# Optimization experiments

Measured on AMD Instinct MI355X. Metric: run time of the kernel, lower is better.

The kernel has to match this reference:

```python
import jax, jax.numpy as jnp
import numpy as np

HEAD_NUM = 16
KEY_DIM = 64
EMBED = 1024
KV_OUT = HEAD_NUM * KEY_DIM  # 1024


def setup_inputs() -> dict:
    key = jax.random.key(0)
    ks = jax.random.split(key, 11)
    B, L, E = 2, 2048, EMBED
    scale = 0.02
    return {
        "query": jax.random.normal(ks[0], (B, L, E), jnp.float32),
        "key": jax.random.normal(ks[1], (B, L, E), jnp.float32),
        "value": jax.random.normal(ks[2], (B, L, E), jnp.float32),
        "W_Query": jax.random.normal(ks[3], (E, KV_OUT), jnp.float32) * scale,
        "W_Key": jax.random.normal(ks[4], (E, KV_OUT), jnp.float32) * scale,
        "W_Value": jax.random.normal(ks[5], (E, KV_OUT), jnp.float32) * scale,
        "W_Output": jax.random.normal(ks[6], (KV_OUT, E), jnp.float32) * scale,
        "B_Query": jnp.zeros((KV_OUT,), jnp.float32),
        "B_Key": jnp.zeros((KV_OUT,), jnp.float32),
        "B_Value": jnp.zeros((KV_OUT,), jnp.float32),
        "B_Output": jnp.zeros((E,), jnp.float32),
    }


def reference(query, key, value, W_Query, W_Key, W_Value, W_Output,
              B_Query, B_Key, B_Value, B_Output):
    B, Lq, E = query.shape
    Lk = key.shape[1]
    H, D = HEAD_NUM, KEY_DIM
    # QKV projections + bias
    q = query @ W_Query + B_Query            # [B, Lq, H*D]
    k = key @ W_Key + B_Key                  # [B, Lk, H*D]
    v = value @ W_Value + B_Value            # [B, Lk, H*D]
    # tf.split(axis=2) per head == reshape to [B, L, H, D]
    q = q.reshape(B, Lq, H, D)
    k = k.reshape(B, Lk, H, D)
    v = v.reshape(B, Lk, H, D)
    # scaled dot-product attention (no mask, dropout=0)
    scores = jnp.einsum("bqhd,bkhd->bhqk", q, k) / (D ** 0.5)
    probs = jax.nn.softmax(scores, axis=-1)
    out = jnp.einsum("bhqk,bkhd->bqhd", probs, v)  # [B, Lq, H, D]
    out = out.reshape(B, Lq, H * D)
    return out @ W_Output + B_Output
```

## Files before the change

### kernel.cpp

```cpp
#include <hip/hip_runtime.h>

using u16 = unsigned short;
using u32 = unsigned int;

typedef __attribute__((ext_vector_type(8))) short bf16x8;
typedef __attribute__((ext_vector_type(4))) float f32x4;
typedef __attribute__((ext_vector_type(4))) u32 u32x4;
typedef __attribute__((ext_vector_type(2))) u32 u32x2;
typedef __attribute__((ext_vector_type(4))) _Float16 f16x4;

#define MFMA_BF16_K32(a, b, c) __builtin_amdgcn_mfma_f32_16x16x32_bf16((a), (b), (c), 0, 0, 0)
#define MFMA_F16_K16(a, b, c) __builtin_amdgcn_mfma_f32_16x16x16f16((a), (b), (c), 0, 0, 0)

#define QSCALE 0.18033688011112042f

extern "C" __device__ float __ocml_native_exp2_f32(float);

__device__ __forceinline__ u16 f2bf(float f) {
  u32 u = __builtin_bit_cast(u32, f);
  return (u16)((u + 0x7fffu + ((u >> 16) & 1u)) >> 16);
}

__device__ __forceinline__ u32 pk_f16(float a, float b) {
  auto v = __builtin_amdgcn_cvt_pkrtz(a, b);
  return __builtin_bit_cast(u32, v);
}

__device__ __forceinline__ void load_lds16(const void* g, void* l) {
  __builtin_amdgcn_global_load_lds((__attribute__((address_space(1))) void*)g,
                                   (__attribute__((address_space(3))) void*)l,
                                   16, 0, 0);
}

__global__ __launch_bounds__(256) void cvt_all_kernel(
    const float* __restrict__ q, const float* __restrict__ k, const float* __restrict__ v,
    u16* __restrict__ oq, u16* __restrict__ ok, u16* __restrict__ ov,
    const float* __restrict__ w0, const float* __restrict__ w1,
    const float* __restrict__ w2, const float* __restrict__ w3,
    u16* __restrict__ d0, u16* __restrict__ d1,
    u16* __restrict__ d2, u16* __restrict__ d3) {
  const int id = blockIdx.x;
  const int tid = threadIdx.x;
  if (id < 6144) {
    const int z = id >> 11, bx = id & 2047;
    const float* s = z == 0 ? q : z == 1 ? k : v;
    u16* d = z == 0 ? oq : z == 1 ? ok : ov;
    int i = (bx * 256 + tid) * 8;
    f32x4 a = *(const f32x4*)(s + i);
    f32x4 b = *(const f32x4*)(s + i + 4);
    u32x4 o;
    o.x = (u32)f2bf(a.x) | ((u32)f2bf(a.y) << 16);
    o.y = (u32)f2bf(a.z) | ((u32)f2bf(a.w) << 16);
    o.z = (u32)f2bf(b.x) | ((u32)f2bf(b.y) << 16);
    o.w = (u32)f2bf(b.z) | ((u32)f2bf(b.w) << 16);
    *(u32x4*)(d + i) = o;
    return;
  }
  __shared__ float t[64][65];
  const int r0 = id - 6144;
  const int z = r0 >> 8, rr0 = r0 & 255;
  const int bx = rr0 & 15, by = rr0 >> 4;
  const float* src = z == 0 ? w0 : z == 1 ? w1 : z == 2 ? w2 : w3;
  u16* dst = z == 0 ? d0 : z == 1 ? d1 : z == 2 ? d2 : d3;
  const float scale = (z == 0) ? QSCALE : 1.0f;
  const int r = tid >> 4, c4 = (tid & 15) * 4;
#pragma unroll
  for (int i = 0; i < 4; ++i) {
    int row = r + i * 16;
    f32x4 vv = *(const f32x4*)(src + (by * 64 + row) * 1024 + bx * 64 + c4);
    t[row][c4 + 0] = vv.x;
    t[row][c4 + 1] = vv.y;
    t[row][c4 + 2] = vv.z;
    t[row][c4 + 3] = vv.w;
  }
  __syncthreads();
  const int rw = tid >> 2, cc = (tid & 3) * 16;
  alignas(16) u16 tmp[16];
#pragma unroll
  for (int j = 0; j < 16; ++j) tmp[j] = f2bf(t[cc + j][rw] * scale);
  u32x4* outp = (u32x4*)(dst + (bx * 64 + rw) * 1024 + by * 64 + cc);
  outp[0] = *(const u32x4*)&tmp[0];
  outp[1] = *(const u32x4*)&tmp[8];
}

__global__ __launch_bounds__(256) void gemm_qkv_kernel(
    const u16* __restrict__ x0, const u16* __restrict__ x1, const u16* __restrict__ x2,
    const u16* __restrict__ w0, const u16* __restrict__ w1, const u16* __restrict__ w2,
    const float* __restrict__ b0, const float* __restrict__ b1, const float* __restrict__ b2,
    u16* __restrict__ c0, u16* __restrict__ c1, u16* __restrict__ vt) {
  __shared__ u16 As[128 * 64];
  __shared__ u16 Bs[128 * 64];
  const int lid = blockIdx.x;
  const int xcd = lid & 7, rr = lid >> 3;
  const int nb = rr & 7, slot = rr >> 3;
  const int g = slot * 8 + xcd;
  const int z = g >> 5, m_idx = g & 31;
  const u16* A = z == 0 ? x0 : z == 1 ? x1 : x2;
  const u16* Bt = z == 0 ? w0 : z == 1 ? w1 : w2;
  const float* bias = z == 0 ? b0 : z == 1 ? b1 : b2;
  const float bscale = z == 0 ? QSCALE : 1.0f;
  const int tid = threadIdx.x;
  const int wave = tid >> 6, lane = tid & 63;
  const int l16 = lane & 15, quad = lane >> 4;
  const int l7 = l16 & 7;
  const int wm = wave >> 1, wn = wave & 1;
  const int m0 = m_idx * 128, n0 = nb * 128;

  f32x4 acc[4][4];
  const f32x4 zf = {0.f, 0.f, 0.f, 0.f};
#pragma unroll
  for (int i = 0; i < 4; ++i)
#pragma unroll
    for (int j = 0; j < 4; ++j) acc[i][j] = zf;

  for (int kb = 0; kb < 1024; kb += 64) {
#pragma unroll
    for (int t = 0; t < 4; ++t) {
      int c = wave * 256 + t * 64 + lane;
      int row = c >> 3, sc8 = (c & 7) ^ (row & 7);
      load_lds16(A + (m0 + row) * 1024 + kb + sc8 * 8, &As[(wave * 256 + t * 64) * 8]);
    }
#pragma unroll
    for (int t = 0; t < 4; ++t) {
      int c = wave * 256 + t * 64 + lane;
      int row = c >> 3, sc8 = (c & 7) ^ (row & 7);
      load_lds16(Bt + (n0 + row) * 1024 + kb + sc8 * 8, &Bs[(wave * 256 + t * 64) * 8]);
    }
    asm volatile("s_waitcnt vmcnt(0)" ::: "memory");
    __syncthreads();
#pragma unroll
    for (int ks = 0; ks < 2; ++ks) {
      const int sch = (ks * 4 + quad) ^ l7;
      bf16x8 af[4], bfv[4];
#pragma unroll
      for (int mt = 0; mt < 4; ++mt)
        af[mt] = *(const bf16x8*)&As[(wm * 64 + mt * 16 + l16) * 64 + sch * 8];
#pragma unroll
      for (int nt = 0; nt < 4; ++nt)
        bfv[nt] = *(const bf16x8*)&Bs[(wn * 64 + nt * 16 + l16) * 64 + sch * 8];
#pragma unroll
      for (int mt = 0; mt < 4; ++mt)
#pragma unroll
        for (int nt = 0; nt < 4; ++nt) acc[mt][nt] = MFMA_BF16_K32(af[mt], bfv[nt], acc[mt][nt]);
    }
    __syncthreads();
  }

  float bv[4];
#pragma unroll
  for (int nt = 0; nt < 4; ++nt) bv[nt] = bias[n0 + wn * 64 + nt * 16 + l16] * bscale;
  if (z != 2) {
    u16* C = z == 0 ? c0 : c1;
#pragma unroll
    for (int mt = 0; mt < 4; ++mt)
#pragma unroll
      for (int nt = 0; nt < 4; ++nt)
#pragma unroll
        for (int r = 0; r < 4; ++r) {
          int row = m0 + wm * 64 + mt * 16 + quad * 4 + r;
          int col = n0 + wn * 64 + nt * 16 + l16;
          C[row * 1024 + col] = f2bf(acc[mt][nt][r] + bv[nt]);
        }
  } else {
#pragma unroll
    for (int mt = 0; mt < 4; ++mt)
#pragma unroll
      for (int nt = 0; nt < 4; ++nt)
#pragma unroll
        for (int r = 0; r < 4; ++r) {
          int row = m0 + wm * 64 + mt * 16 + quad * 4 + r;
          int col = n0 + wn * 64 + nt * 16 + l16;
          int bb = row >> 11, kv = row & 2047;
          _Float16 hv = (_Float16)(acc[mt][nt][r] + bv[nt]);
          vt[(bb * 1024 + col) * 2048 + kv] = __builtin_bit_cast(u16, hv);
        }
  }
}

__global__ __launch_bounds__(256) void gemm_out_kernel(const u16* __restrict__ A,
                                                       const u16* __restrict__ Bt,
                                                       const float* __restrict__ bias,
                                                       float* __restrict__ C) {
  __shared__ u16 As[64 * 64];
  __shared__ u16 Bs[128 * 64];
  const int lid = blockIdx.x;
  const int xcd = lid & 7, rr = lid >> 3;
  const int nb = rr & 7, slot = rr >> 3;
  const int by = slot * 8 + xcd;
  const int tid = threadIdx.x;
  const int wave = tid >> 6, lane = tid & 63;
  const int l16 = lane & 15, quad = lane >> 4;
  const int l7 = l16 & 7;
  const int m0 = by * 64, n0 = nb * 128;

  f32x4 acc[4][2];
  const f32x4 zf = {0.f, 0.f, 0.f, 0.f};
#pragma unroll
  for (int i = 0; i < 4; ++i)
#pragma unroll
    for (int j = 0; j < 2; ++j) acc[i][j] = zf;

  for (int kb = 0; kb < 1024; kb += 64) {
#pragma unroll
    for (int t = 0; t < 2; ++t) {
      int c = wave * 128 + t * 64 + lane;
      int row = c >> 3, sc8 = (c & 7) ^ (row & 7);
      load_lds16(A + (m0 + row) * 1024 + kb + sc8 * 8, &As[(wave * 128 + t * 64) * 8]);
    }
#pragma unroll
    for (int t = 0; t < 4; ++t) {
      int c = wave * 256 + t * 64 + lane;
      int row = c >> 3, sc8 = (c & 7) ^ (row & 7);
      load_lds16(Bt + (n0 + row) * 1024 + kb + sc8 * 8, &Bs[(wave * 256 + t * 64) * 8]);
    }
    asm volatile("s_waitcnt vmcnt(0)" ::: "memory");
    __syncthreads();
#pragma unroll
    for (int ks = 0; ks < 2; ++ks) {
      const int sch = (ks * 4 + quad) ^ l7;
      bf16x8 af[4], bfv[2];
#pragma unroll
      for (int mt = 0; mt < 4; ++mt)
        af[mt] = *(const bf16x8*)&As[(mt * 16 + l16) * 64 + sch * 8];
#pragma unroll
      for (int nt = 0; nt < 2; ++nt)
        bfv[nt] = *(const bf16x8*)&Bs[(wave * 32 + nt * 16 + l16) * 64 + sch * 8];
#pragma unroll
      for (int mt = 0; mt < 4; ++mt)
#pragma unroll
        for (int nt = 0; nt < 2; ++nt) acc[mt][nt] = MFMA_BF16_K32(af[mt], bfv[nt], acc[mt][nt]);
    }
    __syncthreads();
  }

  float bv[2];
#pragma unroll
  for (int nt = 0; nt < 2; ++nt) bv[nt] = bias[n0 + wave * 32 + nt * 16 + l16];
#pragma unroll
  for (int mt = 0; mt < 4; ++mt)
#pragma unroll
    for (int nt = 0; nt < 2; ++nt)
#pragma unroll
      for (int r = 0; r < 4; ++r) {
        int row = m0 + mt * 16 + quad * 4 + r;
        int col = n0 + wave * 32 + nt * 16 + l16;
        C[row * 1024 + col] = acc[mt][nt][r] + bv[nt];
      }
}

__global__ __launch_bounds__(256, 2) void flash_kernel(const u16* __restrict__ Q,
                                                       const u16* __restrict__ K,
                                                       const u16* __restrict__ Vt,
                                                       u16* __restrict__ O) {
  __shared__ u16 k_lds[2][128 * 64];
  __shared__ u16 vt_lds[2][64 * 128];
  __shared__ float lred[4][64];
  __shared__ float lfin[64];
  const int tid = threadIdx.x;
  const int wave = tid >> 6, lane = tid & 63;
  const int l16 = lane & 15, quad = lane >> 4;
  const int l7 = l16 & 7;
  const int id = blockIdx.x;
  const int xcd = id & 7, slot = id >> 3;
  const int pair = xcd * 4 + (slot & 3);
  const int qb = slot >> 2;
  const int b = pair >> 4, h = pair & 15;
  const u16* Qh = Q + (b * 2048 + qb * 64) * 1024 + h * 64;
  const u16* Kh = K + b * 2048 * 1024 + h * 64;
  const u16* Vh = Vt + pair * 64 * 2048;

#pragma unroll
  for (int t = 0; t < 2; ++t) {
    int c = (t * 4 + wave) * 64 + lane;
    int row = c >> 3, sc8 = (c & 7) ^ (row & 7);
    load_lds16(Qh + row * 1024 + sc8 * 8, &k_lds[0][((t * 4 + wave) * 64) * 8]);
  }
  asm volatile("s_waitcnt vmcnt(0)" ::: "memory");
  __syncthreads();
  bf16x8 qf[4][2];
#pragma unroll
  for (int qn = 0; qn < 4; ++qn)
#pragma unroll
    for (int ks = 0; ks < 2; ++ks)
      qf[qn][ks] = *(const bf16x8*)&k_lds[0][(qn * 16 + l16) * 64 + (((ks * 4 + quad) ^ l7)) * 8];
  __syncthreads();

#pragma unroll
  for (int bufi = 0; bufi < 2; ++bufi) {
    const int kv0 = bufi * 128;
#pragma unroll
    for (int t = 0; t < 4; ++t) {
      int c = (t * 4 + wave) * 64 + lane;
      int row = c >> 3, sc8 = (c & 7) ^ (row & 7);
      load_lds16(Kh + (kv0 + row) * 1024 + sc8 * 8, &k_lds[bufi][((t * 4 + wave) * 64) * 8]);
    }
#pragma unroll
    for (int t = 0; t < 4; ++t) {
      int c = (t * 4 + wave) * 64 + lane;
      int d = c >> 4, sc = (c & 15) ^ (d & 15);
      load_lds16(Vh + d * 2048 + kv0 + sc * 8, &vt_lds[bufi][((t * 4 + wave) * 64) * 8]);
    }
  }

  f32x4 o_acc[4][4];
  const f32x4 zf = {0.f, 0.f, 0.f, 0.f};
#pragma unroll
  for (int qn = 0; qn < 4; ++qn)
#pragma unroll
    for (int dt = 0; dt < 4; ++dt) o_acc[qn][dt] = zf;
  float lp[4] = {0.f, 0.f, 0.f, 0.f};

  for (int kb = 0; kb < 16; ++kb) {
    const int cur = kb & 1;
    if (kb < 15)
      asm volatile("s_waitcnt vmcnt(8)" ::: "memory");
    else
      asm volatile("s_waitcnt vmcnt(0)" ::: "memory");
    __builtin_amdgcn_s_barrier();
    asm volatile("" ::: "memory");

#pragma unroll
    for (int c2 = 0; c2 < 2; ++c2) {
      const int chunk = wave * 2 + c2;
      f32x4 s_acc[4];
#pragma unroll
      for (int qn = 0; qn < 4; ++qn) s_acc[qn] = zf;
#pragma unroll
      for (int ks = 0; ks < 2; ++ks) {
        bf16x8 kf =
            *(const bf16x8*)&k_lds[cur][(chunk * 16 + l16) * 64 + ((ks * 4 + quad) ^ l7) * 8];
        __builtin_amdgcn_s_setprio(1);
#pragma unroll
        for (int qn = 0; qn < 4; ++qn) s_acc[qn] = MFMA_BF16_K32(kf, qf[qn][ks], s_acc[qn]);
        __builtin_amdgcn_s_setprio(0);
      }
      union { u32 u[2]; f16x4 v; } pkv[4];
#pragma unroll
      for (int qn = 0; qn < 4; ++qn) {
        float e0 = __ocml_native_exp2_f32(s_acc[qn].x);
        float e1 = __ocml_native_exp2_f32(s_acc[qn].y);
        float e2 = __ocml_native_exp2_f32(s_acc[qn].z);
        float e3 = __ocml_native_exp2_f32(s_acc[qn].w);
        lp[qn] += (e0 + e1) + (e2 + e3);
        pkv[qn].u[0] = pk_f16(e0, e1);
        pkv[qn].u[1] = pk_f16(e2, e3);
      }
#pragma unroll
      for (int dt = 0; dt < 4; ++dt) {
        f16x4 vf = *(const f16x4*)&vt_lds[cur][(dt * 16 + l16) * 128 +
                                               (((chunk * 2 + (quad >> 1)) ^ l16) * 8) +
                                               (quad & 1) * 4];
        __builtin_amdgcn_s_setprio(1);
#pragma unroll
        for (int qn = 0; qn < 4; ++qn)
          o_acc[qn][dt] = MFMA_F16_K16(pkv[qn].v, vf, o_acc[qn][dt]);
        __builtin_amdgcn_s_setprio(0);
      }
    }

    __builtin_amdgcn_s_barrier();
    asm volatile("" ::: "memory");
    if (kb + 2 < 16) {
      const int kv0 = (kb + 2) * 128;
#pragma unroll
      for (int t = 0; t < 4; ++t) {
        int c = (t * 4 + wave) * 64 + lane;
        int row = c >> 3, sc8 = (c & 7) ^ (row & 7);
        load_lds16(Kh + (kv0 + row) * 1024 + sc8 * 8, &k_lds[cur][((t * 4 + wave) * 64) * 8]);
      }
#pragma unroll
      for (int t = 0; t < 4; ++t) {
        int c = (t * 4 + wave) * 64 + lane;
        int d = c >> 4, sc = (c & 15) ^ (d & 15);
        load_lds16(Vh + d * 2048 + kv0 + sc * 8, &vt_lds[cur][((t * 4 + wave) * 64) * 8]);
      }
    }
  }

#pragma unroll
  for (int qn = 0; qn < 4; ++qn) {
    lp[qn] += __shfl_xor(lp[qn], 16);
    lp[qn] += __shfl_xor(lp[qn], 32);
  }
  if (quad == 0) {
#pragma unroll
    for (int qn = 0; qn < 4; ++qn) lred[wave][qn * 16 + l16] = lp[qn];
  }
  float* bufA = (float*)&k_lds[0][0];
  float* bufB = (float*)&k_lds[1][0];
  if (wave == 1 || wave == 3) {
    float* buf = (wave == 1) ? bufA : bufB;
#pragma unroll
    for (int qm = 0; qm < 4; ++qm)
#pragma unroll
      for (int dt = 0; dt < 4; ++dt)
        *(f32x4*)&buf[(((qm * 4 + dt) * 4 + quad) * 16 + l16) * 4] = o_acc[qm][dt];
  }
  __syncthreads();
  if (tid < 64) lfin[tid] = lred[0][tid] + lred[1][tid] + lred[2][tid] + lred[3][tid];
  if (wave == 0 || wave == 2) {
    float* buf = (wave == 0) ? bufA : bufB;
#pragma unroll
    for (int qm = 0; qm < 4; ++qm)
#pragma unroll
      for (int dt = 0; dt < 4; ++dt)
        o_acc[qm][dt] += *(const f32x4*)&buf[(((qm * 4 + dt) * 4 + quad) * 16 + l16) * 4];
  }
  __syncthreads();
  if (wave == 2) {
#pragma unroll
    for (int qm = 0; qm < 4; ++qm)
#pragma unroll
      for (int dt = 0; dt < 4; ++dt)
        *(f32x4*)&bufA[(((qm * 4 + dt) * 4 + quad) * 16 + l16) * 4] = o_acc[qm][dt];
  }
  __syncthreads();
  if (wave == 0) {
#pragma unroll
    for (int qm = 0; qm < 4; ++qm)
#pragma unroll
      for (int dt = 0; dt < 4; ++dt)
        o_acc[qm][dt] += *(const f32x4*)&bufA[(((qm * 4 + dt) * 4 + quad) * 16 + l16) * 4];
#pragma unroll
    for (int qm = 0; qm < 4; ++qm)
#pragma unroll
      for (int r = 0; r < 4; ++r) {
        int qrow = qm * 16 + quad * 4 + r;
        float inv = 1.0f / lfin[qrow];
        int row = b * 2048 + qb * 64 + qrow;
#pragma unroll
        for (int dt = 0; dt < 4; ++dt)
          O[row * 1024 + h * 64 + dt * 16 + l16] = f2bf(o_acc[qm][dt][r] * inv);
      }
  }
}

extern "C" void kernel_launch(void* const* d_in, const int* in_sizes, int n_in,
                              void* d_out, int out_size, void* d_ws, size_t ws_size,
                              hipStream_t stream) {
  const float* q = (const float*)d_in[0];
  const float* k = (const float*)d_in[1];
  const float* v = (const float*)d_in[2];
  const float* Wq = (const float*)d_in[3];
  const float* Wk = (const float*)d_in[4];
  const float* Wv = (const float*)d_in[5];
  const float* Wo = (const float*)d_in[6];
  const float* Bq = (const float*)d_in[7];
  const float* Bk = (const float*)d_in[8];
  const float* Bv = (const float*)d_in[9];
  const float* Bo = (const float*)d_in[10];
  float* out = (float*)d_out;

  char* w = (char*)d_ws;
  const size_t MB = 1u << 20;
  u16* xq = (u16*)(w + 0 * MB);
  u16* xk = (u16*)(w + 8 * MB);
  u16* xv = (u16*)(w + 16 * MB);
  u16* wqt = (u16*)(w + 24 * MB);
  u16* wkt = (u16*)(w + 26 * MB);
  u16* wvt = (u16*)(w + 28 * MB);
  u16* wot = (u16*)(w + 30 * MB);
  u16* Qp = (u16*)(w + 32 * MB);
  u16* Kp = (u16*)(w + 40 * MB);
  u16* Vtr = (u16*)(w + 48 * MB);
  u16* At = (u16*)(w + 56 * MB);

  cvt_all_kernel<<<dim3(7168), 256, 0, stream>>>(q, k, v, xq, xk, xv,
                                                 Wq, Wk, Wv, Wo, wqt, wkt, wvt, wot);
  gemm_qkv_kernel<<<dim3(768), 256, 0, stream>>>(xq, xk, xv, wqt, wkt, wvt,
                                                 Bq, Bk, Bv, Qp, Kp, Vtr);
  flash_kernel<<<dim3(1024), 256, 0, stream>>>(Qp, Kp, Vtr, At);
  gemm_out_kernel<<<dim3(512), 256, 0, stream>>>(At, wot, Bo, out);
}
```

Measured before the change: 231.2 us.

## Pre-tile V^T into MFMA fragment layout and load V directly to registers

The V projection epilogue now writes V^T in a blocked layout that matches the flash kernel's MFMA B-operand fragments, using vectorized 4-element f16 stores. The flash kernel drops the V LDS double buffer and loads V fragments straight from global memory into registers at the start of each KV block, deferring the PV MFMAs until after the next K prefetch is issued. This cuts LDS traffic and capacity and may raise occupancy, at the cost of exposed global-load latency for V within each iteration and more live registers.

```diff
diff --git a/kernel.cpp b/kernel.cpp
--- a/kernel.cpp
+++ b/kernel.cpp
@@ -165,15 +165,19 @@
 #pragma unroll
     for (int mt = 0; mt < 4; ++mt)
 #pragma unroll
-      for (int nt = 0; nt < 4; ++nt)
-#pragma unroll
-        for (int r = 0; r < 4; ++r) {
-          int row = m0 + wm * 64 + mt * 16 + quad * 4 + r;
-          int col = n0 + wn * 64 + nt * 16 + l16;
-          int bb = row >> 11, kv = row & 2047;
-          _Float16 hv = (_Float16)(acc[mt][nt][r] + bv[nt]);
-          vt[(bb * 1024 + col) * 2048 + kv] = __builtin_bit_cast(u16, hv);
-        }
+      for (int nt = 0; nt < 4; ++nt) {
+        int kvb = m0 + wm * 64 + mt * 16 + quad * 4;
+        int bb = kvb >> 11, kv = kvb & 2047;
+        int col = n0 + wn * 64 + nt * 16 + l16;
+        int h = col >> 6, dt = (col >> 4) & 3, ld = col & 15;
+        int pair = bb * 16 + h;
+        int kb2 = kv >> 7, chunk = (kv >> 4) & 7, qd = (kv >> 2) & 3;
+        f16x4 hv;
+#pragma unroll
+        for (int r = 0; r < 4; ++r) hv[r] = (_Float16)(acc[mt][nt][r] + bv[nt]);
+        u16* dst = vt + ((((pair * 16 + kb2) * 8 + chunk) * 4 + dt) * 256) + qd * 64 + ld * 4;
+        *(f16x4*)dst = hv;
+      }
   }
 }
 
@@ -253,7 +257,6 @@
                                                        const u16* __restrict__ Vt,
                                                        u16* __restrict__ O) {
   __shared__ u16 k_lds[2][128 * 64];
-  __shared__ u16 vt_lds[2][64 * 128];
   __shared__ float lred[4][64];
   __shared__ float lfin[64];
   const int tid = threadIdx.x;
@@ -267,7 +270,7 @@
   const int b = pair >> 4, h = pair & 15;
   const u16* Qh = Q + (b * 2048 + qb * 64) * 1024 + h * 64;
   const u16* Kh = K + b * 2048 * 1024 + h * 64;
-  const u16* Vh = Vt + pair * 64 * 2048;
+  const u16* Vh = Vt + pair * 131072;
 
 #pragma unroll
   for (int t = 0; t < 2; ++t) {
@@ -287,18 +290,12 @@
 
 #pragma unroll
   for (int bufi = 0; bufi < 2; ++bufi) {
-    const int kv0 = bufi * 128;
 #pragma unroll
     for (int t = 0; t < 4; ++t) {
       int c = (t * 4 + wave) * 64 + lane;
       int row = c >> 3, sc8 = (c & 7) ^ (row & 7);
-      load_lds16(Kh + (kv0 + row) * 1024 + sc8 * 8, &k_lds[bufi][((t * 4 + wave) * 64) * 8]);
-    }
-#pragma unroll
-    for (int t = 0; t < 4; ++t) {
-      int c = (t * 4 + wave) * 64 + lane;
-      int d = c >> 4, sc = (c & 15) ^ (d & 15);
-      load_lds16(Vh + d * 2048 + kv0 + sc * 8, &vt_lds[bufi][((t * 4 + wave) * 64) * 8]);
+      load_lds16(Kh + (bufi * 128 + row) * 1024 + sc8 * 8,
+                 &k_lds[bufi][((t * 4 + wave) * 64) * 8]);
     }
   }
 
@@ -312,13 +309,21 @@
 
   for (int kb = 0; kb < 16; ++kb) {
     const int cur = kb & 1;
-    if (kb < 15)
-      asm volatile("s_waitcnt vmcnt(8)" ::: "memory");
-    else
-      asm volatile("s_waitcnt vmcnt(0)" ::: "memory");
+    if (kb == 0) asm volatile("s_waitcnt vmcnt(4)" ::: "memory");
     __builtin_amdgcn_s_barrier();
     asm volatile("" ::: "memory");
 
+    const u16* vp = Vh + kb * 8192;
+    f16x4 vreg[2][4];
+#pragma unroll
+    for (int c2 = 0; c2 < 2; ++c2) {
+      const int chunk = wave * 2 + c2;
+#pragma unroll
+      for (int dt = 0; dt < 4; ++dt)
+        vreg[c2][dt] = *(const f16x4*)(vp + (chunk * 4 + dt) * 256 + lane * 4);
+    }
+
+    union { u32 u[2]; f16x4 v; } pkv[2][4];
 #pragma unroll
     for (int c2 = 0; c2 < 2; ++c2) {
       const int chunk = wave * 2 + c2;
@@ -334,7 +339,6 @@
         for (int qn = 0; qn < 4; ++qn) s_acc[qn] = MFMA_BF16_K32(kf, qf[qn][ks], s_acc[qn]);
         __builtin_amdgcn_s_setprio(0);
       }
-      union { u32 u[2]; f16x4 v; } pkv[4];
 #pragma unroll
       for (int qn = 0; qn < 4; ++qn) {
         float e0 = __ocml_native_exp2_f32(s_acc[qn].x);
@@ -342,24 +346,15 @@
         float e2 = __ocml_native_exp2_f32(s_acc[qn].z);
         float e3 = __ocml_native_exp2_f32(s_acc[qn].w);
         lp[qn] += (e0 + e1) + (e2 + e3);
-        pkv[qn].u[0] = pk_f16(e0, e1);
-        pkv[qn].u[1] = pk_f16(e2, e3);
-      }
-#pragma unroll
-      for (int dt = 0; dt < 4; ++dt) {
-        f16x4 vf = *(const f16x4*)&vt_lds[cur][(dt * 16 + l16) * 128 +
-                                               (((chunk * 2 + (quad >> 1)) ^ l16) * 8) +
-                                               (quad & 1) * 4];
-        __builtin_amdgcn_s_setprio(1);
-#pragma unroll
-        for (int qn = 0; qn < 4; ++qn)
-          o_acc[qn][dt] = MFMA_F16_K16(pkv[qn].v, vf, o_acc[qn][dt]);
-        __builtin_amdgcn_s_setprio(0);
-      }
-    }
-
+        pkv[c2][qn].u[0] = pk_f16(e0, e1);
+        pkv[c2][qn].u[1] = pk_f16(e2, e3);
+      }
+    }
+
+    asm volatile("s_waitcnt lgkmcnt(0)" ::: "memory");
     __builtin_amdgcn_s_barrier();
     asm volatile("" ::: "memory");
+
     if (kb + 2 < 16) {
       const int kv0 = (kb + 2) * 128;
 #pragma unroll
@@ -368,11 +363,21 @@
         int row = c >> 3, sc8 = (c & 7) ^ (row & 7);
         load_lds16(Kh + (kv0 + row) * 1024 + sc8 * 8, &k_lds[cur][((t * 4 + wave) * 64) * 8]);
       }
-#pragma unroll
-      for (int t = 0; t < 4; ++t) {
-        int c = (t * 4 + wave) * 64 + lane;
-        int d = c >> 4, sc = (c & 15) ^ (d & 15);
-        load_lds16(Vh + d * 2048 + kv0 + sc * 8, &vt_lds[cur][((t * 4 + wave) * 64) * 8]);
+    }
+    if (kb < 14)
+      asm volatile("s_waitcnt vmcnt(4)" ::: "memory");
+    else
+      asm volatile("s_waitcnt vmcnt(0)" ::: "memory");
+
+#pragma unroll
+    for (int c2 = 0; c2 < 2; ++c2) {
+#pragma unroll
+      for (int dt = 0; dt < 4; ++dt) {
+        __builtin_amdgcn_s_setprio(1);
+#pragma unroll
+        for (int qn = 0; qn < 4; ++qn)
+          o_acc[qn][dt] = MFMA_F16_K16(pkv[c2][qn].v, vreg[c2][dt], o_acc[qn][dt]);
+        __builtin_amdgcn_s_setprio(0);
       }
     }
   }
```

New measurement: 229.6 us. Within noise of the previous version (-0.7%).
